# Performance work log

Measured on AMD Instinct MI355X. Metric: run time of the kernel, lower is better.

Reference implementation:

```python
import jax, jax.numpy as jnp
import numpy as np

H_RATIO = 0.33  # matches init_kwargs h_ratio
EPS = 1e-12     # F.normalize default eps


def setup_inputs() -> dict:
    key = jax.random.key(0)
    x = jax.random.normal(key, (64, 2048, 24, 12), dtype=jnp.float32)
    return {"x": x}


def reference(x):
    b, c, h, w = x.shape
    rh = round(H_RATIO * h)  # number of top-energy rows to drop (static)
    # per-sample spatial activation energy, summed over channels: (b, h*w)
    act = jnp.sum(x * x, axis=1).reshape(b, h * w)
    # L2 normalize per sample (faithful to F.normalize; order-preserving anyway)
    norm = jnp.sqrt(jnp.sum(act * act, axis=1, keepdims=True))
    act = act / jnp.maximum(norm, EPS)
    act = act.reshape(b, h, w)
    # per-row max over width -> (b, h); take indices of the rh largest rows
    max_act = jnp.max(act, axis=2)
    ind = jnp.argsort(max_act, axis=1)[:, -rh:]  # (b, rh)
    # row mask: ones everywhere, zero at the top-rh rows per sample
    mask = jnp.ones((b, h), dtype=x.dtype)
    mask = mask.at[jnp.arange(b)[:, None], ind].set(0.0)  # (b, h)
    # broadcast over channels and width (equiv. to the repeat_interleave chain)
    return x * mask[:, None, :, None]
```

## Files before the change

### kernel.cpp

```cpp
#include <hip/hip_runtime.h>

#define B   64
#define C   2048
#define H   24
#define W   12
#define S   (H * W)
#define S4  (S / 4)
#define W4  (W / 4)
#define NCH 32
#define CCH (C / NCH)
#define RH  8

typedef float f4 __attribute__((ext_vector_type(4)));

__global__ __launch_bounds__(288) void k_energy(const float* __restrict__ x,
                                                float* __restrict__ part) {
    const int chunk = blockIdx.x;
    const int b     = blockIdx.y;
    const int t     = threadIdx.x;
    const int f     = t % S4;
    const int g     = t / S4;

    const f4* __restrict__ x4 =
        (const f4*)x + (size_t)(b * C + chunk * CCH) * S4;

    f4 acc = {0.f, 0.f, 0.f, 0.f};
    #pragma unroll
    for (int k = 0; k < CCH / 4; ++k) {
        f4 v = x4[t + S * k];
        acc += v * v;
    }

    __shared__ f4 sm4[4][S4];
    sm4[g][f] = acc;
    __syncthreads();

    const float* sm = (const float*)sm4;
    part[((size_t)b * NCH + chunk) * S + t] =
        sm[0 * S + t] + sm[1 * S + t] + sm[2 * S + t] + sm[3 * S + t];
}

__global__ __launch_bounds__(288) void k_select(const float* __restrict__ part,
                                                int* __restrict__ drop) {
    const int b = blockIdx.x;
    const int t = threadIdx.x;

    __shared__ float act[S];
    __shared__ float rm[H];

    const float* p = part + (size_t)b * NCH * S + t;
    float sum = 0.f;
    #pragma unroll
    for (int ch = 0; ch < NCH; ch++) sum += p[(size_t)ch * S];
    act[t] = sum;
    __syncthreads();

    if (t < H) {
        float m = act[t * W];
        #pragma unroll
        for (int w = 1; w < W; w++) m = fmaxf(m, act[t * W + w]);
        rm[t] = m;
    }
    __syncthreads();

    if (t < H) {
        const float mt = rm[t];
        int cnt = 0;
        #pragma unroll
        for (int j = 0; j < H; j++) {
            float mj = rm[j];
            if (mj > mt || (mj == mt && j > t)) cnt++;
        }
        drop[b * H + t] = (cnt < RH) ? 1 : 0;
    }
}

__global__ __launch_bounds__(288) void k_mask_copy(const float* __restrict__ x,
                                                   float* __restrict__ out,
                                                   const int* __restrict__ drop) {
    const int chunk = blockIdx.x;
    const int b     = blockIdx.y;
    const int t     = threadIdx.x;
    const int h     = (t % S4) / W4;
    const float keep = (drop[b * H + h] == 0) ? 1.0f : 0.0f;

    const size_t base4 = (size_t)(b * C + chunk * CCH) * S4;
    const f4* __restrict__ x4 = (const f4*)x + base4;
    f4* __restrict__       o4 = (f4*)out + base4;

    #pragma unroll
    for (int k = 0; k < CCH / 4; ++k) {
        f4 v = x4[t + S * k];
        f4 r = v * keep;
        __builtin_nontemporal_store(r, &o4[t + S * k]);
    }
}

extern "C" void kernel_launch(void* const* d_in, const int* in_sizes, int n_in,
                              void* d_out, int out_size, void* d_ws, size_t ws_size,
                              hipStream_t stream) {
    const float* x   = (const float*)d_in[0];
    float*       out = (float*)d_out;

    float* part = (float*)d_ws;
    int*   drop = (int*)((char*)d_ws + (size_t)B * NCH * S * sizeof(float));

    k_energy<<<dim3(NCH, B), 288, 0, stream>>>(x, part);
    k_select<<<B, 288, 0, stream>>>(part, drop);
    k_mask_copy<<<dim3(NCH, B), 288, 0, stream>>>(x, out, drop);
}
```

Measured before the change: 276.8 us.

## Fuse row selection into masked copy kernel and skip reads for dropped rows

The separate select kernel is removed. Every copy block now recomputes the per-sample row energies from the partial sums, ranks the rows, and masks them itself, so one launch and the global drop array go away. Dropped rows are written as zeros without reading x, which removes about a third of the input reads in the copy pass. In exchange, each of the 32 chunk blocks per sample redundantly reads the 32x288 partials and does the small top-k step, adding latency and extra traffic at the start of every block.

```diff
diff --git a/kernel.cpp b/kernel.cpp
--- a/kernel.cpp
+++ b/kernel.cpp
@@ -40,19 +40,24 @@
         sm[0 * S + t] + sm[1 * S + t] + sm[2 * S + t] + sm[3 * S + t];
 }
 
-__global__ __launch_bounds__(288) void k_select(const float* __restrict__ part,
-                                                int* __restrict__ drop) {
-    const int b = blockIdx.x;
-    const int t = threadIdx.x;
+__global__ __launch_bounds__(288) void k_select_copy(const float* __restrict__ x,
+                                                     const float* __restrict__ part,
+                                                     float* __restrict__ out) {
+    const int chunk = blockIdx.x;
+    const int b     = blockIdx.y;
+    const int t     = threadIdx.x;
 
     __shared__ float act[S];
     __shared__ float rm[H];
+    __shared__ int   keepRow[H];
 
-    const float* p = part + (size_t)b * NCH * S + t;
-    float sum = 0.f;
-    #pragma unroll
-    for (int ch = 0; ch < NCH; ch++) sum += p[(size_t)ch * S];
-    act[t] = sum;
+    {
+        const float* p = part + (size_t)b * NCH * S + t;
+        float sum = 0.f;
+        #pragma unroll
+        for (int ch = 0; ch < NCH; ch++) sum += p[(size_t)ch * S];
+        act[t] = sum;
+    }
     __syncthreads();
 
     if (t < H) {
@@ -71,28 +76,27 @@
             float mj = rm[j];
             if (mj > mt || (mj == mt && j > t)) cnt++;
         }
-        drop[b * H + t] = (cnt < RH) ? 1 : 0;
+        keepRow[t] = (cnt < RH) ? 0 : 1;
     }
-}
+    __syncthreads();
 
-__global__ __launch_bounds__(288) void k_mask_copy(const float* __restrict__ x,
-                                                   float* __restrict__ out,
-                                                   const int* __restrict__ drop) {
-    const int chunk = blockIdx.x;
-    const int b     = blockIdx.y;
-    const int t     = threadIdx.x;
-    const int h     = (t % S4) / W4;
-    const float keep = (drop[b * H + h] == 0) ? 1.0f : 0.0f;
-
+    const int h = (t % S4) / W4;
     const size_t base4 = (size_t)(b * C + chunk * CCH) * S4;
     const f4* __restrict__ x4 = (const f4*)x + base4;
     f4* __restrict__       o4 = (f4*)out + base4;
 
-    #pragma unroll
-    for (int k = 0; k < CCH / 4; ++k) {
-        f4 v = x4[t + S * k];
-        f4 r = v * keep;
-        __builtin_nontemporal_store(r, &o4[t + S * k]);
+    if (keepRow[h]) {
+        #pragma unroll
+        for (int k = 0; k < CCH / 4; ++k) {
+            f4 v = x4[t + S * k];
+            __builtin_nontemporal_store(v, &o4[t + S * k]);
+        }
+    } else {
+        const f4 z = {0.f, 0.f, 0.f, 0.f};
+        #pragma unroll
+        for (int k = 0; k < CCH / 4; ++k) {
+            __builtin_nontemporal_store(z, &o4[t + S * k]);
+        }
     }
 }
 
@@ -103,9 +107,7 @@
     float*       out = (float*)d_out;
 
     float* part = (float*)d_ws;
-    int*   drop = (int*)((char*)d_ws + (size_t)B * NCH * S * sizeof(float));
 
     k_energy<<<dim3(NCH, B), 288, 0, stream>>>(x, part);
-    k_select<<<B, 288, 0, stream>>>(part, drop);
-    k_mask_copy<<<dim3(NCH, B), 288, 0, stream>>>(x, out, drop);
+    k_select_copy<<<dim3(NCH, B), 288, 0, stream>>>(x, part, out);
 }
```

Result: slower. 321.7 us (+16.2%).
